# Kernel optimization log

Measured on AMD Instinct MI355X. Metric: run time of the kernel, lower is better.

Reference implementation:

```python
import jax, jax.numpy as jnp
import numpy as np

N = 100000      # nodes
E = 1600000     # directed edges (avg degree 16)
F_IN = 256      # in_feats
H = 4           # num_heads
D = 32          # n_hidden per head
NEG_SLOPE = 0.2


def setup_inputs() -> dict:
    key = jax.random.key(0)
    k_feat, k_src, k_dst, k_perm, k_w, k_a = jax.random.split(key, 6)
    features = jax.random.normal(k_feat, (N, F_IN), dtype=jnp.float32)
    src = jax.random.randint(k_src, (E,), 0, N, dtype=jnp.int32)
    dst = jax.random.randint(k_dst, (E,), 0, N, dtype=jnp.int32)
    # fixed instance of torch.randperm(N) for the corrupt=True gather
    perm = jax.random.permutation(k_perm, N).astype(jnp.int32)
    W = jax.random.normal(k_w, (F_IN, H * D), dtype=jnp.float32) / np.sqrt(F_IN)
    a = jax.random.normal(k_a, (2, H, D), dtype=jnp.float32) * 0.1
    return dict(features=features, W=W, attn_l=a[0], attn_r=a[1],
                src=src, dst=dst, perm=perm)


def reference(features, W, attn_l, attn_r, src, dst, perm):
    # corrupt=True path: node-permutation gather
    x = features[perm]                                  # [N, F_IN]
    # GAT layer: shared linear projection -> [N, H, D]
    h = (x @ W).reshape(N, H, D)
    # per-node attention half-scores
    el = jnp.sum(h * attn_l, axis=-1)                   # [N, H]
    er = jnp.sum(h * attn_r, axis=-1)                   # [N, H]
    # per-edge raw attention (gather)
    e = jax.nn.leaky_relu(el[src] + er[dst], NEG_SLOPE)  # [E, H]
    # softmax over edges grouped by destination node (segment softmax)
    emax = jax.ops.segment_max(e, dst, num_segments=N)  # [N, H]
    ee = jnp.exp(e - emax[dst])                         # [E, H]
    denom = jax.ops.segment_sum(ee, dst, num_segments=N)  # [N, H]
    alpha = ee / denom[dst]                             # [E, H]
    # weighted neighbor aggregation (gather-scale-scatter)
    msg = h[src] * alpha[:, :, None]                    # [E, H, D]
    out = jax.ops.segment_sum(msg, dst, num_segments=N)  # [N, H, D]
    return jax.nn.elu(out.reshape(N, H * D))            # [N, 128]
```

## Files before the change

kernel.cpp:

```cpp
#include <hip/hip_runtime.h>
#include <hip/hip_bf16.h>
#include <math.h>

#define N_NODES 100000
#define E_EDGES 1600000
#define F_IN    256
#define HD      128
#define NHEAD   4
#define DHEAD   32
#define NEG_SLOPE 0.2f
#define CAP     64
#define NBIN    200
#define BINW    500
#define CHUNK   8192
#define NCHUNK  196
#define BINCAP  16384
#define GEMMBLK 782

typedef __attribute__((ext_vector_type(8))) __bf16 bf16x8;
typedef __attribute__((ext_vector_type(4))) float  f32x4;
typedef __attribute__((ext_vector_type(8))) unsigned short u16x8;

__device__ __forceinline__ unsigned short f2bf(float x) {
    unsigned int b = __float_as_uint(x);
    b += 0x7fffu + ((b >> 16) & 1u);
    return (unsigned short)(b >> 16);
}
__device__ __forceinline__ float bf2f(unsigned short u) {
    return __uint_as_float((unsigned int)u << 16);
}

__global__ void k_prep(const float* __restrict__ W, unsigned short* __restrict__ wbf) {
    int i = blockIdx.x * 256 + threadIdx.x;
    if (i >= F_IN * HD) return;
    int k = i >> 7, c = i & 127;
    unsigned short v = f2bf(W[i]);
    *(unsigned short*)((char*)wbf + (size_t)c * 512 + ((2 * k) ^ ((c & 7) << 4))) = v;
}

__global__ __launch_bounds__(256) void k_fat1(const float* __restrict__ X,
        const unsigned short* __restrict__ wbf, const int* __restrict__ perm,
        unsigned short* __restrict__ hb,
        const int* __restrict__ src, const int* __restrict__ dst,
        int* __restrict__ cursor, unsigned int* __restrict__ binbuf) {
    __shared__ __align__(16) unsigned char smem[65536];
    const int tid = threadIdx.x;

    if (blockIdx.x < NCHUNK) {
        unsigned int*  buf     = (unsigned int*)smem;
        unsigned char* binid   = smem + 32768;
        unsigned int*  hist    = (unsigned int*)(smem + 40960);
        unsigned int*  pfx     = (unsigned int*)(smem + 41792);
        unsigned int*  base_sh = (unsigned int*)(smem + 42624);
        unsigned int*  cnt2    = (unsigned int*)(smem + 43456);
        const int e0 = blockIdx.x * CHUNK;
        const int n = min(CHUNK, E_EDGES - e0);

        for (int i = tid; i < NBIN; i += 256) { hist[i] = 0; cnt2[i] = 0; }
        __syncthreads();
        for (int i = tid; i < n; i += 256) {
            int d = dst[e0 + i];
            atomicAdd(&hist[d / BINW], 1u);
        }
        __syncthreads();
        if (tid < NBIN) pfx[tid] = hist[tid];
        __syncthreads();
        for (int off = 1; off < NBIN; off <<= 1) {
            unsigned v = (tid < NBIN) ? pfx[tid] : 0;
            unsigned u = (tid >= off && tid < NBIN) ? pfx[tid - off] : 0;
            __syncthreads();
            if (tid < NBIN) pfx[tid] = v + u;
            __syncthreads();
        }
        if (tid < NBIN) base_sh[tid] = (unsigned)atomicAdd(cursor + tid, (int)hist[tid]);
        __syncthreads();
        for (int i = tid; i < n; i += 256) {
            int d = dst[e0 + i];
            int s = src[e0 + i];
            int b = d / BINW;
            unsigned pos = atomicAdd(&cnt2[b], 1u);
            unsigned idx = pfx[b] - hist[b] + pos;
            buf[idx] = ((unsigned)(d - b * BINW) << 17) | (unsigned)s;
            binid[idx] = (unsigned char)b;
        }
        __syncthreads();
        for (int i = tid; i < n; i += 256) {
            int b = binid[i];
            unsigned ex = pfx[b] - hist[b];
            unsigned gpos = base_sh[b] + ((unsigned)i - ex);
            if (gpos < BINCAP) binbuf[(long)b * BINCAP + gpos] = buf[i];
        }
    } else {
        unsigned short* Bs = (unsigned short*)smem;
        {
            const float4* srcv = (const float4*)wbf;
            float4* dstv = (float4*)Bs;
#pragma unroll
            for (int i = 0; i < 16; i++) dstv[tid + i * 256] = srcv[tid + i * 256];
        }
        __syncthreads();

        const int bid = blockIdx.x - NCHUNK;
        const int l   = tid & 63;
        const int wv  = tid >> 6;
        const int l15 = l & 15;
        const int kg  = l >> 4;
        const int rowbase = bid * 128 + wv * 32;

        int r0 = rowbase + l15;      if (r0 >= N_NODES) r0 = N_NODES - 1;
        int r1 = rowbase + 16 + l15; if (r1 >= N_NODES) r1 = N_NODES - 1;
        const float* aptr0 = X + (long)perm[r0] * F_IN + kg * 8;
        const float* aptr1 = X + (long)perm[r1] * F_IN + kg * 8;

        f32x4 acc[2][8];
#pragma unroll
        for (int rt = 0; rt < 2; rt++)
#pragma unroll
            for (int ct = 0; ct < 8; ct++) acc[rt][ct] = (f32x4){0.f, 0.f, 0.f, 0.f};

#pragma unroll
        for (int k0 = 0; k0 < F_IN; k0 += 32) {
            bf16x8 a0, a1;
            {
                float4 v0 = *(const float4*)(aptr0 + k0);
                float4 v1 = *(const float4*)(aptr0 + k0 + 4);
                a0[0]=(__bf16)v0.x; a0[1]=(__bf16)v0.y; a0[2]=(__bf16)v0.z; a0[3]=(__bf16)v0.w;
                a0[4]=(__bf16)v1.x; a0[5]=(__bf16)v1.y; a0[6]=(__bf16)v1.z; a0[7]=(__bf16)v1.w;
            }
            {
                float4 v0 = *(const float4*)(aptr1 + k0);
                float4 v1 = *(const float4*)(aptr1 + k0 + 4);
                a1[0]=(__bf16)v0.x; a1[1]=(__bf16)v0.y; a1[2]=(__bf16)v0.z; a1[3]=(__bf16)v0.w;
                a1[4]=(__bf16)v1.x; a1[5]=(__bf16)v1.y; a1[6]=(__bf16)v1.z; a1[7]=(__bf16)v1.w;
            }
            const int sb = k0 * 2 + kg * 16;
#pragma unroll
            for (int ct = 0; ct < 8; ct++) {
                int c = ct * 16 + l15;
                bf16x8 b = *(const bf16x8*)((const char*)Bs + c * 512 + (sb ^ ((c & 7) << 4)));
                acc[0][ct] = __builtin_amdgcn_mfma_f32_16x16x32_bf16(a0, b, acc[0][ct], 0, 0, 0);
                acc[1][ct] = __builtin_amdgcn_mfma_f32_16x16x32_bf16(a1, b, acc[1][ct], 0, 0, 0);
            }
        }

#pragma unroll
        for (int rt = 0; rt < 2; rt++)
#pragma unroll
            for (int i = 0; i < 4; i++) {
                int row = rowbase + rt * 16 + kg * 4 + i;
                if (row < N_NODES) {
                    unsigned short* op = hb + (long)row * HD + l15;
#pragma unroll
                    for (int ct = 0; ct < 8; ct++) op[ct * 16] = f2bf(acc[rt][ct][i]);
                }
            }
    }
}

__global__ __launch_bounds__(256) void k_fat2(const unsigned int* __restrict__ binbuf,
        const int* __restrict__ cursor, int* __restrict__ cnt, int* __restrict__ bucket,
        const unsigned short* __restrict__ hb, const float* __restrict__ al,
        const float* __restrict__ ar, float* __restrict__ el, float* __restrict__ er) {
    __shared__ int cnt_l[BINW];
    if (blockIdx.x < NBIN) {
        const int b = blockIdx.x;
        const int n = min(cursor[b], BINCAP);
        for (int i = threadIdx.x; i < BINW; i += 256) cnt_l[i] = 0;
        __syncthreads();
        const unsigned int* bp = binbuf + (long)b * BINCAP;
        for (int i = threadIdx.x; i < n; i += 256) {
            unsigned p = bp[i];
            int dl = (int)(p >> 17);
            int s  = (int)(p & 0x1FFFFu);
            int pos = atomicAdd(&cnt_l[dl], 1);
            if (pos < CAP) bucket[((long)b * BINW + dl) * CAP + pos] = s;
        }
        __syncthreads();
        for (int i = threadIdx.x; i < BINW; i += 256) cnt[b * BINW + i] = cnt_l[i];
    } else {
        int i = (blockIdx.x - NBIN) * 256 + threadIdx.x;
        if (i >= N_NODES * NHEAD) return;
        int head = i & 3;
        const unsigned short* hp = hb + (long)i * DHEAD;
        float sl = 0.f, sr = 0.f;
#pragma unroll
        for (int j = 0; j < 8; j++) {
            ushort4 hv = *(const ushort4*)(hp + j * 4);
            float4 a = *(const float4*)(al + head * DHEAD + j * 4);
            float4 b = *(const float4*)(ar + head * DHEAD + j * 4);
            sl += bf2f(hv.x) * a.x + bf2f(hv.y) * a.y + bf2f(hv.z) * a.z + bf2f(hv.w) * a.w;
            sr += bf2f(hv.x) * b.x + bf2f(hv.y) * b.y + bf2f(hv.z) * b.z + bf2f(hv.w) * b.w;
        }
        el[i] = sl;
        er[i] = sr;
    }
}

__global__ __launch_bounds__(256) void k_aggr(const float* __restrict__ el,
        const float* __restrict__ er, const int* __restrict__ cnt,
        const int* __restrict__ bucket, const unsigned short* __restrict__ hb,
        float* __restrict__ out) {
    int wid = (int)((blockIdx.x * (long)blockDim.x + threadIdx.x) >> 6);
    if (wid >= N_NODES) return;
    const int lane = threadIdx.x & 63;
    const int g    = lane >> 4;
    const int l4   = lane & 15;
    const int head = l4 >> 2;
    int deg = cnt[wid];
    if (deg > CAP) deg = CAP;
    const float ern = er[(long)wid * 4 + head];
    int myS = (lane < deg) ? bucket[(long)wid * CAP + lane] : 0;
    float acc[8];
#pragma unroll
    for (int j = 0; j < 8; j++) acc[j] = 0.f;
    float asum = 0.f;
    for (int i = 0; i < deg; i += 4) {
        int e = i + g;
        int s = __shfl(myS, e & 63, 64);
        u16x8 hv = *(const u16x8*)(hb + (long)s * HD + l4 * 8);
        float a = 0.f;
        if (e < deg) {
            float v = el[(long)s * 4 + head] + ern;
            v = v > 0.f ? v : NEG_SLOPE * v;
            a = __expf(v);
        }
        asum += a;
#pragma unroll
        for (int j = 0; j < 8; j++) acc[j] += bf2f(hv[j]) * a;
    }
#pragma unroll
    for (int off = 16; off <= 32; off <<= 1) {
        asum += __shfl_xor(asum, off, 64);
#pragma unroll
        for (int j = 0; j < 8; j++) acc[j] += __shfl_xor(acc[j], off, 64);
    }
    if (g == 0) {
        float inv = asum > 0.f ? 1.f / asum : 0.f;
        float4 o0, o1;
        float t;
        t = acc[0] * inv; o0.x = t > 0.f ? t : __expf(t) - 1.f;
        t = acc[1] * inv; o0.y = t > 0.f ? t : __expf(t) - 1.f;
        t = acc[2] * inv; o0.z = t > 0.f ? t : __expf(t) - 1.f;
        t = acc[3] * inv; o0.w = t > 0.f ? t : __expf(t) - 1.f;
        t = acc[4] * inv; o1.x = t > 0.f ? t : __expf(t) - 1.f;
        t = acc[5] * inv; o1.y = t > 0.f ? t : __expf(t) - 1.f;
        t = acc[6] * inv; o1.z = t > 0.f ? t : __expf(t) - 1.f;
        t = acc[7] * inv; o1.w = t > 0.f ? t : __expf(t) - 1.f;
        float* op = out + (long)wid * HD + l4 * 8;
        *(float4*)op = o0;
        *(float4*)(op + 4) = o1;
    }
}

extern "C" void kernel_launch(void* const* d_in, const int* in_sizes, int n_in,
                              void* d_out, int out_size, void* d_ws, size_t ws_size,
                              hipStream_t stream) {
    const float* features = (const float*)d_in[0];
    const float* W        = (const float*)d_in[1];
    const float* attn_l   = (const float*)d_in[2];
    const float* attn_r   = (const float*)d_in[3];
    const int*   src      = (const int*)d_in[4];
    const int*   dst      = (const int*)d_in[5];
    const int*   perm     = (const int*)d_in[6];
    float* out = (float*)d_out;

    char* ws = (char*)d_ws;
    const size_t OFF_HB   = 0;
    const size_t OFF_EL   = 25600000;
    const size_t OFF_ER   = 27200000;
    const size_t OFF_CNT  = 28800000;
    const size_t OFF_CUR  = 29200000;
    const size_t OFF_WBF  = 29204096;
    const size_t OFF_BKT  = 29269632;
    const size_t OFF_BINB = 54869632;

    unsigned short* hb    = (unsigned short*)(ws + OFF_HB);
    float* el     = (float*)(ws + OFF_EL);
    float* er     = (float*)(ws + OFF_ER);
    int*   cnt    = (int*)(ws + OFF_CNT);
    int*   cursor = (int*)(ws + OFF_CUR);
    unsigned short* wbf = (unsigned short*)(ws + OFF_WBF);
    int*   bucket = (int*)(ws + OFF_BKT);
    unsigned int* binbuf = (unsigned int*)(ws + OFF_BINB);

    hipMemsetAsync(ws + OFF_CUR, 0, 4096, stream);

    k_prep<<<(F_IN * HD + 255) / 256, 256, 0, stream>>>(W, wbf);
    k_fat1<<<NCHUNK + GEMMBLK, 256, 0, stream>>>(features, wbf, perm, hb,
                                                 src, dst, cursor, binbuf);
    k_fat2<<<NBIN + (N_NODES * NHEAD + 255) / 256, 256, 0, stream>>>(
        binbuf, cursor, cnt, bucket, hb, attn_l, attn_r, el, er);
    k_aggr<<<(N_NODES * 64 + 255) / 256, 256, 0, stream>>>(el, er, cnt, bucket, hb, out);
}
```

Measured before the change: 147.4 us.

## Fold attention vectors into GEMM weights and split GEMM across both fat kernels

The attention dot products are precomputed into W (W·attn_l and W·attn_r become 8 extra output columns), so the GEMM writes el/er directly and the separate per-node attention pass is dropped. The GEMM blocks are also split between k_fat1 and k_fat2 so each half overlaps with a different binning phase. This adds an extra MFMA column tile and more shared memory per block, which can lower occupancy. It also computes el/er from bf16-rounded folded weights rather than from rounded h, which changes the numerics slightly.

```diff
diff --git a/kernel.cpp b/kernel.cpp
--- a/kernel.cpp
+++ b/kernel.cpp
@@ -15,7 +15,10 @@
 #define CHUNK   8192
 #define NCHUNK  196
 #define BINCAP  16384
-#define GEMMBLK 782
+#define NC      144
+#define NCT     9
+#define GEMS1   392
+#define GEMS2   390
 
 typedef __attribute__((ext_vector_type(8))) __bf16 bf16x8;
 typedef __attribute__((ext_vector_type(4))) float  f32x4;
@@ -30,20 +33,105 @@
     return __uint_as_float((unsigned int)u << 16);
 }
 
-__global__ void k_prep(const float* __restrict__ W, unsigned short* __restrict__ wbf) {
-    int i = blockIdx.x * 256 + threadIdx.x;
-    if (i >= F_IN * HD) return;
-    int k = i >> 7, c = i & 127;
-    unsigned short v = f2bf(W[i]);
-    *(unsigned short*)((char*)wbf + (size_t)c * 512 + ((2 * k) ^ ((c & 7) << 4))) = v;
+__global__ void k_prep(const float* __restrict__ W, const float* __restrict__ al,
+                       const float* __restrict__ ar, unsigned short* __restrict__ wbf) {
+    const int k = blockIdx.x;
+    const int c = threadIdx.x;
+    float v;
+    if (c < 128) {
+        v = W[k * HD + c];
+    } else if (c < 132) {
+        int h = c - 128; float s = 0.f;
+        for (int d = 0; d < DHEAD; d++) s += W[k * HD + h * DHEAD + d] * al[h * DHEAD + d];
+        v = s;
+    } else if (c < 136) {
+        int h = c - 132; float s = 0.f;
+        for (int d = 0; d < DHEAD; d++) s += W[k * HD + h * DHEAD + d] * ar[h * DHEAD + d];
+        v = s;
+    } else {
+        v = 0.f;
+    }
+    *(unsigned short*)((char*)wbf + (size_t)c * 512 + ((2 * k) ^ ((c & 7) << 4))) = f2bf(v);
+}
+
+__device__ __forceinline__ void gemm_role(int bid, int tid,
+        unsigned char* smem, const float* __restrict__ X,
+        const unsigned short* __restrict__ wbf, const int* __restrict__ perm,
+        unsigned short* __restrict__ hb, float* __restrict__ el,
+        float* __restrict__ er) {
+    unsigned short* Bs = (unsigned short*)smem;
+    {
+        const float4* srcv = (const float4*)wbf;
+        float4* dstv = (float4*)Bs;
+#pragma unroll
+        for (int i = 0; i < 18; i++) dstv[tid + i * 256] = srcv[tid + i * 256];
+    }
+    __syncthreads();
+
+    const int l   = tid & 63;
+    const int wv  = tid >> 6;
+    const int l15 = l & 15;
+    const int kg  = l >> 4;
+    const int rowbase = bid * 128 + wv * 32;
+
+    int r0 = rowbase + l15;      if (r0 >= N_NODES) r0 = N_NODES - 1;
+    int r1 = rowbase + 16 + l15; if (r1 >= N_NODES) r1 = N_NODES - 1;
+    const float* aptr0 = X + (long)perm[r0] * F_IN + kg * 8;
+    const float* aptr1 = X + (long)perm[r1] * F_IN + kg * 8;
+
+    f32x4 acc[2][NCT];
+#pragma unroll
+    for (int rt = 0; rt < 2; rt++)
+#pragma unroll
+        for (int ct = 0; ct < NCT; ct++) acc[rt][ct] = (f32x4){0.f, 0.f, 0.f, 0.f};
+
+#pragma unroll
+    for (int k0 = 0; k0 < F_IN; k0 += 32) {
+        bf16x8 a0, a1;
+        {
+            float4 v0 = *(const float4*)(aptr0 + k0);
+            float4 v1 = *(const float4*)(aptr0 + k0 + 4);
+            a0[0]=(__bf16)v0.x; a0[1]=(__bf16)v0.y; a0[2]=(__bf16)v0.z; a0[3]=(__bf16)v0.w;
+            a0[4]=(__bf16)v1.x; a0[5]=(__bf16)v1.y; a0[6]=(__bf16)v1.z; a0[7]=(__bf16)v1.w;
+        }
+        {
+            float4 v0 = *(const float4*)(aptr1 + k0);
+            float4 v1 = *(const float4*)(aptr1 + k0 + 4);
+            a1[0]=(__bf16)v0.x; a1[1]=(__bf16)v0.y; a1[2]=(__bf16)v0.z; a1[3]=(__bf16)v0.w;
+            a1[4]=(__bf16)v1.x; a1[5]=(__bf16)v1.y; a1[6]=(__bf16)v1.z; a1[7]=(__bf16)v1.w;
+        }
+        const int sb = k0 * 2 + kg * 16;
+#pragma unroll
+        for (int ct = 0; ct < NCT; ct++) {
+            int c = ct * 16 + l15;
+            bf16x8 b = *(const bf16x8*)((const char*)Bs + c * 512 + (sb ^ ((c & 7) << 4)));
+            acc[0][ct] = __builtin_amdgcn_mfma_f32_16x16x32_bf16(a0, b, acc[0][ct], 0, 0, 0);
+            acc[1][ct] = __builtin_amdgcn_mfma_f32_16x16x32_bf16(a1, b, acc[1][ct], 0, 0, 0);
+        }
+    }
+
+#pragma unroll
+    for (int rt = 0; rt < 2; rt++)
+#pragma unroll
+        for (int i = 0; i < 4; i++) {
+            int row = rowbase + rt * 16 + kg * 4 + i;
+            if (row < N_NODES) {
+                unsigned short* op = hb + (long)row * HD + l15;
+#pragma unroll
+                for (int ct = 0; ct < 8; ct++) op[ct * 16] = f2bf(acc[rt][ct][i]);
+                float v = acc[rt][8][i];
+                if (l15 < 4)      el[(long)row * 4 + l15]       = v;
+                else if (l15 < 8) er[(long)row * 4 + (l15 - 4)] = v;
+            }
+        }
 }
 
 __global__ __launch_bounds__(256) void k_fat1(const float* __restrict__ X,
         const unsigned short* __restrict__ wbf, const int* __restrict__ perm,
-        unsigned short* __restrict__ hb,
+        unsigned short* __restrict__ hb, float* __restrict__ el, float* __restrict__ er,
         const int* __restrict__ src, const int* __restrict__ dst,
         int* __restrict__ cursor, unsigned int* __restrict__ binbuf) {
-    __shared__ __align__(16) unsigned char smem[65536];
+    __shared__ __align__(16) unsigned char smem[73728];
     const int tid = threadIdx.x;
 
     if (blockIdx.x < NCHUNK) {
@@ -91,78 +179,18 @@
             if (gpos < BINCAP) binbuf[(long)b * BINCAP + gpos] = buf[i];
         }
     } else {
-        unsigned short* Bs = (unsigned short*)smem;
-        {
-            const float4* srcv = (const float4*)wbf;
-            float4* dstv = (float4*)Bs;
-#pragma unroll
-            for (int i = 0; i < 16; i++) dstv[tid + i * 256] = srcv[tid + i * 256];
-        }
-        __syncthreads();
-
-        const int bid = blockIdx.x - NCHUNK;
-        const int l   = tid & 63;
-        const int wv  = tid >> 6;
-        const int l15 = l & 15;
-        const int kg  = l >> 4;
-        const int rowbase = bid * 128 + wv * 32;
-
-        int r0 = rowbase + l15;      if (r0 >= N_NODES) r0 = N_NODES - 1;
-        int r1 = rowbase + 16 + l15; if (r1 >= N_NODES) r1 = N_NODES - 1;
-        const float* aptr0 = X + (long)perm[r0] * F_IN + kg * 8;
-        const float* aptr1 = X + (long)perm[r1] * F_IN + kg * 8;
-
-        f32x4 acc[2][8];
-#pragma unroll
-        for (int rt = 0; rt < 2; rt++)
-#pragma unroll
-            for (int ct = 0; ct < 8; ct++) acc[rt][ct] = (f32x4){0.f, 0.f, 0.f, 0.f};
-
-#pragma unroll
-        for (int k0 = 0; k0 < F_IN; k0 += 32) {
-            bf16x8 a0, a1;
-            {
-                float4 v0 = *(const float4*)(aptr0 + k0);
-                float4 v1 = *(const float4*)(aptr0 + k0 + 4);
-                a0[0]=(__bf16)v0.x; a0[1]=(__bf16)v0.y; a0[2]=(__bf16)v0.z; a0[3]=(__bf16)v0.w;
-                a0[4]=(__bf16)v1.x; a0[5]=(__bf16)v1.y; a0[6]=(__bf16)v1.z; a0[7]=(__bf16)v1.w;
-            }
-            {
-                float4 v0 = *(const float4*)(aptr1 + k0);
-                float4 v1 = *(const float4*)(aptr1 + k0 + 4);
-                a1[0]=(__bf16)v0.x; a1[1]=(__bf16)v0.y; a1[2]=(__bf16)v0.z; a1[3]=(__bf16)v0.w;
-                a1[4]=(__bf16)v1.x; a1[5]=(__bf16)v1.y; a1[6]=(__bf16)v1.z; a1[7]=(__bf16)v1.w;
-            }
-            const int sb = k0 * 2 + kg * 16;
-#pragma unroll
-            for (int ct = 0; ct < 8; ct++) {
-                int c = ct * 16 + l15;
-                bf16x8 b = *(const bf16x8*)((const char*)Bs + c * 512 + (sb ^ ((c & 7) << 4)));
-                acc[0][ct] = __builtin_amdgcn_mfma_f32_16x16x32_bf16(a0, b, acc[0][ct], 0, 0, 0);
-                acc[1][ct] = __builtin_amdgcn_mfma_f32_16x16x32_bf16(a1, b, acc[1][ct], 0, 0, 0);
-            }
-        }
-
-#pragma unroll
-        for (int rt = 0; rt < 2; rt++)
-#pragma unroll
-            for (int i = 0; i < 4; i++) {
-                int row = rowbase + rt * 16 + kg * 4 + i;
-                if (row < N_NODES) {
-                    unsigned short* op = hb + (long)row * HD + l15;
-#pragma unroll
-                    for (int ct = 0; ct < 8; ct++) op[ct * 16] = f2bf(acc[rt][ct][i]);
-                }
-            }
+        gemm_role(blockIdx.x - NCHUNK, tid, smem, X, wbf, perm, hb, el, er);
     }
 }
 
 __global__ __launch_bounds__(256) void k_fat2(const unsigned int* __restrict__ binbuf,
         const int* __restrict__ cursor, int* __restrict__ cnt, int* __restrict__ bucket,
-        const unsigned short* __restrict__ hb, const float* __restrict__ al,
-        const float* __restrict__ ar, float* __restrict__ el, float* __restrict__ er) {
-    __shared__ int cnt_l[BINW];
+        const float* __restrict__ X, const unsigned short* __restrict__ wbf,
+        const int* __restrict__ perm, unsigned short* __restrict__ hb,
+        float* __restrict__ el, float* __restrict__ er) {
+    __shared__ __align__(16) unsigned char smem[73728];
     if (blockIdx.x < NBIN) {
+        int* cnt_l = (int*)smem;
         const int b = blockIdx.x;
         const int n = min(cursor[b], BINCAP);
         for (int i = threadIdx.x; i < BINW; i += 256) cnt_l[i] = 0;
@@ -178,21 +206,8 @@
         __syncthreads();
         for (int i = threadIdx.x; i < BINW; i += 256) cnt[b * BINW + i] = cnt_l[i];
     } else {
-        int i = (blockIdx.x - NBIN) * 256 + threadIdx.x;
-        if (i >= N_NODES * NHEAD) return;
-        int head = i & 3;
-        const unsigned short* hp = hb + (long)i * DHEAD;
-        float sl = 0.f, sr = 0.f;
-#pragma unroll
-        for (int j = 0; j < 8; j++) {
-            ushort4 hv = *(const ushort4*)(hp + j * 4);
-            float4 a = *(const float4*)(al + head * DHEAD + j * 4);
-            float4 b = *(const float4*)(ar + head * DHEAD + j * 4);
-            sl += bf2f(hv.x) * a.x + bf2f(hv.y) * a.y + bf2f(hv.z) * a.z + bf2f(hv.w) * a.w;
-            sr += bf2f(hv.x) * b.x + bf2f(hv.y) * b.y + bf2f(hv.z) * b.z + bf2f(hv.w) * b.w;
-        }
-        el[i] = sl;
-        er[i] = sr;
+        gemm_role(GEMS1 + (blockIdx.x - NBIN), threadIdx.x, smem, X, wbf, perm,
+                  hb, el, er);
     }
 }
 
@@ -271,8 +286,8 @@
     const size_t OFF_CNT  = 28800000;
     const size_t OFF_CUR  = 29200000;
     const size_t OFF_WBF  = 29204096;
-    const size_t OFF_BKT  = 29269632;
-    const size_t OFF_BINB = 54869632;
+    const size_t OFF_BKT  = 29286016;
+    const size_t OFF_BINB = 54886016;
 
     unsigned short* hb    = (unsigned short*)(ws + OFF_HB);
     float* el     = (float*)(ws + OFF_EL);
@@ -285,10 +300,10 @@
 
     hipMemsetAsync(ws + OFF_CUR, 0, 4096, stream);
 
-    k_prep<<<(F_IN * HD + 255) / 256, 256, 0, stream>>>(W, wbf);
-    k_fat1<<<NCHUNK + GEMMBLK, 256, 0, stream>>>(features, wbf, perm, hb,
-                                                 src, dst, cursor, binbuf);
-    k_fat2<<<NBIN + (N_NODES * NHEAD + 255) / 256, 256, 0, stream>>>(
-        binbuf, cursor, cnt, bucket, hb, attn_l, attn_r, el, er);
+    k_prep<<<F_IN, NC, 0, stream>>>(W, attn_l, attn_r, wbf);
+    k_fat1<<<NCHUNK + GEMS1, 256, 0, stream>>>(features, wbf, perm, hb, el, er,
+                                               src, dst, cursor, binbuf);
+    k_fat2<<<NBIN + GEMS2, 256, 0, stream>>>(binbuf, cursor, cnt, bucket,
+                                             features, wbf, perm, hb, el, er);
     k_aggr<<<(N_NODES * 64 + 255) / 256, 256, 0, stream>>>(el, er, cnt, bucket, hb, out);
 }
```

Result: faster. 142.7 us (-3.2%).
